# Optimization experiments

Hardware: AMD Instinct MI355X
Metric: run time of the kernel (lower is better)

The kernel has to match this reference:

```python
import jax, jax.numpy as jnp
import numpy as np

NUM_HEADS = 32
NUM_KV = 8
HEAD_DIM = 128


def rotate_half(x):
    half = x.shape[-1] // 2
    x1, x2 = x[..., :half], x[..., half:]
    return jnp.concatenate([-x2, x1], axis=-1)


def apply_rope(x, cos, sin):
    # x: [B, H, S, D]; cos/sin: [S, D] broadcast over batch and heads
    return x * cos + rotate_half(x) * sin


def setup_inputs() -> dict:
    key = jax.random.key(0)
    kx, kqkv, kout = jax.random.split(key, 3)
    B, S, H = 2, 2048, 4096
    x = jax.random.normal(kx, (B, S, H), dtype=jnp.float32)
    Wqkv = jax.random.normal(kqkv, (H, NUM_HEADS * HEAD_DIM + 2 * NUM_KV * HEAD_DIM), dtype=jnp.float32) * (H ** -0.5)
    Wout = jax.random.normal(kout, (H, H), dtype=jnp.float32) * (H ** -0.5)
    # realistic RoPE tables (seq, head_dim)
    inv_freq = 1.0 / (10000.0 ** (np.arange(0, HEAD_DIM, 2, dtype=np.float32) / HEAD_DIM))
    freqs = np.outer(np.arange(S, dtype=np.float32), inv_freq)  # [S, D/2]
    emb = np.concatenate([freqs, freqs], axis=-1)  # [S, D]
    cos = jnp.asarray(np.cos(emb), dtype=jnp.float32)
    sin = jnp.asarray(np.sin(emb), dtype=jnp.float32)
    return {"x": x, "cos": cos, "sin": sin, "Wqkv": Wqkv, "Wout": Wout}


def reference(x, cos, sin, Wqkv, Wout):
    B, S, H = x.shape
    nh, nkv, hd = NUM_HEADS, NUM_KV, HEAD_DIM
    qkv = x @ Wqkv  # [B, S, (nh+2*nkv)*hd]
    q, k, v = jnp.split(qkv, [nh * hd, nh * hd + nkv * hd], axis=-1)
    q = q.reshape(B, S, nh, hd).transpose(0, 2, 1, 3)   # [B, nh, S, hd]
    k = k.reshape(B, S, nkv, hd).transpose(0, 2, 1, 3)  # [B, nkv, S, hd]
    v = v.reshape(B, S, nkv, hd).transpose(0, 2, 1, 3)
    q = apply_rope(q, cos, sin)
    k = apply_rope(k, cos, sin)
    group = nh // nkv
    k = jnp.repeat(k, group, axis=1)  # repeat_interleave over head dim
    v = jnp.repeat(v, group, axis=1)
    scale = 1.0 / jnp.sqrt(jnp.asarray(hd, dtype=x.dtype))
    scores = jnp.einsum('bhqd,bhkd->bhqk', q, k) * scale  # [B, nh, S, S]
    causal = jnp.triu(jnp.ones((S, S), dtype=bool), k=1)
    scores = jnp.where(causal, -jnp.inf, scores)
    w = jax.nn.softmax(scores, axis=-1)
    out = jnp.einsum('bhqk,bhkd->bhqd', w, v)  # [B, nh, S, hd]
    out = out.transpose(0, 2, 1, 3).reshape(B, S, nh * hd)
    return out @ Wout
```

## Files before the change

### kernel.cpp

```cpp
#include <hip/hip_runtime.h>

typedef unsigned short u16;
typedef __attribute__((ext_vector_type(8))) short s16x8;
typedef __attribute__((ext_vector_type(4))) short s16x4;
typedef __attribute__((ext_vector_type(4))) float f32x4;

#define DEVI __device__ __forceinline__

DEVI u16 f2b(float f) {
  union { float f; unsigned u; } v; v.f = f;
  unsigned r = v.u + 0x7FFFu + ((v.u >> 16) & 1u);
  return (u16)(r >> 16);
}
DEVI float b2f(u16 h) {
  union { unsigned u; float f; } v; v.u = ((unsigned)h) << 16;
  return v.f;
}

typedef const __attribute__((address_space(1))) void gas_void;
typedef __attribute__((address_space(3))) void las_void;
DEVI void gload16(const void* g, void* l) {
  __builtin_amdgcn_global_load_lds((gas_void*)g, (las_void*)l, 16, 0, 0);
}

__global__ void conv_bf16(const float* __restrict__ in, u16* __restrict__ out, int n8) {
  int i = blockIdx.x * 256 + threadIdx.x;
  if (i >= n8) return;
  const float* p = in + (size_t)i * 8;
  float4 u = *(const float4*)p;
  float4 v = *(const float4*)(p + 4);
  s16x8 o = {(short)f2b(u.x), (short)f2b(u.y), (short)f2b(u.z), (short)f2b(u.w),
             (short)f2b(v.x), (short)f2b(v.y), (short)f2b(v.z), (short)f2b(v.w)};
  *(s16x8*)(out + (size_t)i * 8) = o;
}

__global__ void trans_bf16(const float* __restrict__ W, u16* __restrict__ Wt, int K, int N) {
  __shared__ __attribute__((aligned(16))) u16 tile[64][68];
  const int t = threadIdx.x;
  const int n0 = blockIdx.x * 64, k0 = blockIdx.y * 64;
#pragma unroll
  for (int i = 0; i < 4; ++i) {
    int c = i * 256 + t;
    int r = c >> 4, q = c & 15;
    float4 v = *(const float4*)(W + (size_t)(k0 + r) * N + n0 + q * 4);
    s16x4 o = {(short)f2b(v.x), (short)f2b(v.y), (short)f2b(v.z), (short)f2b(v.w)};
    *(s16x4*)&tile[r][q * 4] = o;
  }
  __syncthreads();
#pragma unroll
  for (int i = 0; i < 2; ++i) {
    int c = i * 256 + t;
    int n_ = c >> 3, ck = (c & 7) * 8;
    s16x8 o;
#pragma unroll
    for (int j = 0; j < 8; ++j) o[j] = (short)tile[ck + j][n_];
    *(s16x8*)(Wt + (size_t)(n0 + n_) * K + k0 + ck) = o;
  }
}

template <typename TC>
__global__ __launch_bounds__(512, 2) void gemm256(const u16* __restrict__ A,
                                                  const u16* __restrict__ Bt,
                                                  TC* __restrict__ C, int M, int N, int K) {
  __shared__ __attribute__((aligned(16))) u16 As[2][2][128 * 64];
  __shared__ __attribute__((aligned(16))) u16 Bs[2][2][128 * 64];
  const int t = threadIdx.x;
  const int nbn = N >> 8;
  const int nwg = (M >> 8) * nbn;
  const int chunk = nwg >> 3;
  const int id = (blockIdx.x & 7) * chunk + (blockIdx.x >> 3);
  const int row0 = (id / nbn) << 8, col0 = (id % nbn) << 8;
  const int w = t >> 6, lane = t & 63, lc = lane & 15, lg = lane >> 4;
  const int wqm = (w >> 2) * 64;
  const int wqn = (w & 3) * 32;
  const int sw7 = lc & 7;

  const f32x4 FZ = {0.f, 0.f, 0.f, 0.f};
  f32x4 acc[4][4][2];
#pragma unroll
  for (int q = 0; q < 4; ++q)
#pragma unroll
    for (int i = 0; i < 4; ++i)
#pragma unroll
      for (int j = 0; j < 2; ++j) acc[q][i][j] = FZ;

  const int s_r0 = t >> 3, s_r1 = (512 + t) >> 3;
  const int s_s = t & 7;

#define STG_A(kt, H, sl)                                                                   \
  {                                                                                        \
    gload16(A + (size_t)(row0 + (H)*128 + s_r0) * K + ((kt) << 6) + ((s_s ^ (s_r0 & 7)) << 3), \
            (u16*)As[sl][H] + t * 8);                                                      \
    gload16(A + (size_t)(row0 + (H)*128 + s_r1) * K + ((kt) << 6) + ((s_s ^ (s_r1 & 7)) << 3), \
            (u16*)As[sl][H] + (512 + t) * 8);                                              \
  }
#define STG_B(kt, H, sl)                                                                   \
  {                                                                                        \
    gload16(Bt + (size_t)(col0 + (H)*128 + s_r0) * K + ((kt) << 6) + ((s_s ^ (s_r0 & 7)) << 3), \
            (u16*)Bs[sl][H] + t * 8);                                                      \
    gload16(Bt + (size_t)(col0 + (H)*128 + s_r1) * K + ((kt) << 6) + ((s_s ^ (s_r1 & 7)) << 3), \
            (u16*)Bs[sl][H] + (512 + t) * 8);                                              \
  }
#define LOAD_A(MH, buf)                                                           \
  _Pragma("unroll") for (int mf = 0; mf < 4; ++mf)                                \
  _Pragma("unroll") for (int ks = 0; ks < 2; ++ks)                                \
    af[mf][ks] = *(const s16x8*)(As[buf][MH] + (wqm + mf * 16 + lc) * 64 +        \
                                 (((ks * 4 + lg) ^ sw7) << 3));
#define LOAD_B(NH, buf, DST)                                                      \
  _Pragma("unroll") for (int nf = 0; nf < 2; ++nf)                                \
  _Pragma("unroll") for (int ks = 0; ks < 2; ++ks)                                \
    DST[nf][ks] = *(const s16x8*)(Bs[buf][NH] + (wqn + nf * 16 + lc) * 64 +       \
                                  (((ks * 4 + lg) ^ sw7) << 3));
#define MFMA_Q(q, BV)                                                             \
  _Pragma("unroll") for (int ks = 0; ks < 2; ++ks)                                \
  _Pragma("unroll") for (int mf = 0; mf < 4; ++mf)                                \
  _Pragma("unroll") for (int nf = 0; nf < 2; ++nf)                                \
    acc[q][mf][nf] = __builtin_amdgcn_mfma_f32_16x16x32_bf16(                     \
        af[mf][ks], BV[nf][ks], acc[q][mf][nf], 0, 0, 0);
#define BAR __builtin_amdgcn_s_barrier()
#define PRIO1 __builtin_amdgcn_s_setprio(1)
#define PRIO0 __builtin_amdgcn_s_setprio(0)
#define WAIT6 asm volatile("s_waitcnt vmcnt(6)" ::: "memory")

  s16x8 af[4][2], bfv0[2][2], bfv1[2][2];
  const int NT = K >> 6, TM = NT - 1;

  STG_A(0, 0, 0) STG_B(0, 0, 0) STG_B(0, 1, 0) STG_A(0, 1, 0)
  STG_A(1, 0, 1) STG_B(1, 0, 1) STG_B(1, 1, 1)
  WAIT6;
  BAR;

  for (int kt = 0; kt < NT; ++kt) {
    const int buf = kt & 1, nb = buf ^ 1;
    const int tp1 = (kt + 1) & TM, tp2 = (kt + 2) & TM;
    LOAD_A(0, buf) LOAD_B(0, buf, bfv0)
    STG_A(tp1, 1, nb)
    BAR; PRIO1; MFMA_Q(0, bfv0) PRIO0; BAR;
    LOAD_B(1, buf, bfv1)
    STG_A(tp2, 0, buf)
    BAR; PRIO1; MFMA_Q(1, bfv1) PRIO0; BAR;
    LOAD_A(1, buf)
    STG_B(tp2, 0, buf)
    BAR; PRIO1; MFMA_Q(2, bfv1) PRIO0; BAR;
    STG_B(tp2, 1, buf)
    BAR; PRIO1; MFMA_Q(3, bfv0) PRIO0;
    WAIT6;
    BAR;
  }
  asm volatile("s_waitcnt vmcnt(0)" ::: "memory");
  BAR;
#undef STG_A
#undef STG_B
#undef LOAD_A
#undef LOAD_B
#undef MFMA_Q
#undef BAR
#undef PRIO1
#undef PRIO0
#undef WAIT6

  const int qmh[4] = {0, 0, 1, 1}, qnh[4] = {0, 1, 1, 0};
#pragma unroll
  for (int q = 0; q < 4; ++q)
#pragma unroll
    for (int mf = 0; mf < 4; ++mf)
#pragma unroll
      for (int nf = 0; nf < 2; ++nf)
#pragma unroll
        for (int r = 0; r < 4; ++r) {
          const int rg = row0 + qmh[q] * 128 + wqm + mf * 16 + lg * 4 + r;
          const int cg = col0 + qnh[q] * 128 + wqn + nf * 16 + lc;
          if constexpr (sizeof(TC) == 2)
            ((u16*)C)[(size_t)rg * N + cg] = f2b(acc[q][mf][nf][r]);
          else
            ((float*)C)[(size_t)rg * N + cg] = acc[q][mf][nf][r];
        }
}

__global__ void rope_kernel(u16* __restrict__ qkv, const float* __restrict__ cosb,
                            const float* __restrict__ sinb) {
  const int bs = blockIdx.x;
  const int s = bs & 2047;
  u16* row = qkv + (size_t)bs * 6144;
  const float* cr = cosb + s * 128;
  const float* sr = sinb + s * 128;
  for (int p = threadIdx.x; p < 320; p += 256) {
    int head = p >> 3, dc = (p & 7) * 8;
    int ci = head * 128 + dc;
    s16x8 a = *(const s16x8*)&row[ci];
    s16x8 bb = *(const s16x8*)&row[ci + 64];
    float4 c0 = *(const float4*)(cr + dc), c1 = *(const float4*)(cr + dc + 4);
    float4 s0 = *(const float4*)(sr + dc), s1 = *(const float4*)(sr + dc + 4);
    float cv[8] = {c0.x, c0.y, c0.z, c0.w, c1.x, c1.y, c1.z, c1.w};
    float sv[8] = {s0.x, s0.y, s0.z, s0.w, s1.x, s1.y, s1.z, s1.w};
    s16x8 o1, o2;
#pragma unroll
    for (int j = 0; j < 8; ++j) {
      float x1 = b2f((u16)a[j]), x2 = b2f((u16)bb[j]);
      o1[j] = (short)f2b(x1 * cv[j] - x2 * sv[j]);
      o2[j] = (short)f2b(x2 * cv[j] + x1 * sv[j]);
    }
    *(s16x8*)&row[ci] = o1;
    *(s16x8*)&row[ci + 64] = o2;
  }
}

__global__ void vtrans_kernel(const u16* __restrict__ qkv, u16* __restrict__ v_t) {
  __shared__ __attribute__((aligned(16))) u16 tile[64][72];
  const int t = threadIdx.x;
  const int s0 = blockIdx.x * 64;
  const int d0 = blockIdx.y * 64;
  const int bk = blockIdx.z;
  const int b = bk >> 3, kvh = bk & 7;
  const int slot = t & 7, r0 = t >> 3;
#pragma unroll
  for (int i = 0; i < 2; ++i) {
    int s_ = r0 + 32 * i;
    *(s16x8*)&tile[s_][slot * 8] =
        *(const s16x8*)(qkv + (size_t)(b * 2048 + s0 + s_) * 6144 + 5120 + kvh * 128 + d0 + slot * 8);
  }
  __syncthreads();
#pragma unroll
  for (int i = 0; i < 2; ++i) {
    int d_ = r0 + 32 * i;
    s16x8 v;
#pragma unroll
    for (int j = 0; j < 8; ++j) v[j] = (short)tile[slot * 8 + j][d_];
    *(s16x8*)(v_t + ((size_t)bk * 128 + d0 + d_) * 2048 + s0 + slot * 8) = v;
  }
}

__global__ void __launch_bounds__(256, 2) attn_kernel(const u16* __restrict__ qkv,
                                                      const u16* __restrict__ v_t,
                                                      u16* __restrict__ attn) {
  __shared__ __attribute__((aligned(16))) u16 Ks[64][136];
  __shared__ __attribute__((aligned(16))) u16 Vs[128][72];
  __shared__ __attribute__((aligned(16))) u16 Ps[4][32][72];
  const int t = threadIdx.x;
  const int f = blockIdx.x;
  const int xcd = f & 7, ix = f >> 3;
  const int g = (xcd << 1) | (ix >> 6);
  const int r_ = ix & 63;
  const int b = g >> 3, kvh = g & 7;
  const int qt = 15 - (r_ >> 2);
  const int h = kvh * 4 + (r_ & 3);
  const int q0 = qt * 128;
  const int w = t >> 6, lane = t & 63, lc = lane & 15, lg = lane >> 4;
  const int qw = q0 + w * 32;

  const u16* qbase = qkv + (size_t)(b * 2048) * 6144 + h * 128;
  const u16* kbase = qkv + (size_t)(b * 2048) * 6144 + 4096 + kvh * 128;
  const u16* vbase = v_t + (size_t)(b * 8 + kvh) * 128 * 2048;

  s16x8 qf[2][4];
#pragma unroll
  for (int mf = 0; mf < 2; ++mf)
#pragma unroll
    for (int ks = 0; ks < 4; ++ks)
      qf[mf][ks] = *(const s16x8*)(qbase + (size_t)(qw + mf * 16 + lc) * 6144 + ks * 32 + lg * 8);

  const f32x4 FZ = {0.f, 0.f, 0.f, 0.f};
  f32x4 o_acc[2][8];
  float m_run[2][4], l_run[2][4];
#pragma unroll
  for (int mf = 0; mf < 2; ++mf) {
#pragma unroll
    for (int nf = 0; nf < 8; ++nf) o_acc[mf][nf] = FZ;
#pragma unroll
    for (int r = 0; r < 4; ++r) { m_run[mf][r] = -3e38f; l_run[mf][r] = 0.f; }
  }
  const float scale2 = 0.08838834764831845f * 1.44269504088896340736f;

  const int ntiles = q0 / 64 + 2;
  s16x8 kr[4], vr[4];
#pragma unroll
  for (int i = 0; i < 4; ++i) {
    int c = i * 256 + t;
    kr[i] = *(const s16x8*)(kbase + (size_t)(c >> 4) * 6144 + (c & 15) * 8);
    vr[i] = *(const s16x8*)(vbase + (size_t)(c >> 3) * 2048 + (c & 7) * 8);
  }

  for (int kt = 0; kt < ntiles; ++kt) {
    const int k0 = kt * 64;
    __syncthreads();
#pragma unroll
    for (int i = 0; i < 4; ++i) {
      int c = i * 256 + t;
      *(s16x8*)&Ks[c >> 4][(c & 15) * 8] = kr[i];
      *(s16x8*)&Vs[c >> 3][(c & 7) * 8] = vr[i];
    }
    __syncthreads();
    if (kt + 1 < ntiles) {
      int k1 = k0 + 64;
#pragma unroll
      for (int i = 0; i < 4; ++i) {
        int c = i * 256 + t;
        kr[i] = *(const s16x8*)(kbase + (size_t)(k1 + (c >> 4)) * 6144 + (c & 15) * 8);
        vr[i] = *(const s16x8*)(vbase + (size_t)(c >> 3) * 2048 + k1 + (c & 7) * 8);
      }
    }
    if (k0 > qw + 31) continue;

    f32x4 sacc[2][4];
#pragma unroll
    for (int mf = 0; mf < 2; ++mf)
#pragma unroll
      for (int nf = 0; nf < 4; ++nf) sacc[mf][nf] = FZ;
#pragma unroll
    for (int ks = 0; ks < 4; ++ks) {
      s16x8 kf[4];
#pragma unroll
      for (int nf = 0; nf < 4; ++nf)
        kf[nf] = *(const s16x8*)&Ks[nf * 16 + lc][ks * 32 + lg * 8];
#pragma unroll
      for (int mf = 0; mf < 2; ++mf)
#pragma unroll
        for (int nf = 0; nf < 4; ++nf)
          sacc[mf][nf] = __builtin_amdgcn_mfma_f32_16x16x32_bf16(qf[mf][ks], kf[nf], sacc[mf][nf], 0, 0, 0);
    }

#pragma unroll
    for (int mf = 0; mf < 2; ++mf) {
      float pm[4] = {-3e38f, -3e38f, -3e38f, -3e38f};
      const bool dm = (k0 + 63 > qw + mf * 16);
      if (dm) {
#pragma unroll
        for (int nf = 0; nf < 4; ++nf) {
          int kv = k0 + nf * 16 + lc;
#pragma unroll
          for (int r = 0; r < 4; ++r) {
            int qg = qw + mf * 16 + lg * 4 + r;
            float sv = sacc[mf][nf][r] * scale2;
            sv = (kv <= qg) ? sv : -3e38f;
            sacc[mf][nf][r] = sv;
            pm[r] = fmaxf(pm[r], sv);
          }
        }
      } else {
#pragma unroll
        for (int nf = 0; nf < 4; ++nf)
#pragma unroll
          for (int r = 0; r < 4; ++r) {
            float sv = sacc[mf][nf][r] * scale2;
            sacc[mf][nf][r] = sv;
            pm[r] = fmaxf(pm[r], sv);
          }
      }
#pragma unroll
      for (int r = 0; r < 4; ++r) {
        pm[r] = fmaxf(pm[r], __shfl_xor(pm[r], 1));
        pm[r] = fmaxf(pm[r], __shfl_xor(pm[r], 2));
        pm[r] = fmaxf(pm[r], __shfl_xor(pm[r], 4));
        pm[r] = fmaxf(pm[r], __shfl_xor(pm[r], 8));
      }
      bool any = false;
      float mnew[4];
#pragma unroll
      for (int r = 0; r < 4; ++r) {
        mnew[r] = fmaxf(m_run[mf][r], pm[r]);
        any |= (mnew[r] > m_run[mf][r]);
      }
      if (__any(any)) {
#pragma unroll
        for (int r = 0; r < 4; ++r) {
          float fsc = exp2f(m_run[mf][r] - mnew[r]);
          m_run[mf][r] = mnew[r];
          l_run[mf][r] *= fsc;
#pragma unroll
          for (int nf = 0; nf < 8; ++nf) o_acc[mf][nf][r] *= fsc;
        }
      }
      float psum[4] = {0.f, 0.f, 0.f, 0.f};
#pragma unroll
      for (int nf = 0; nf < 4; ++nf)
#pragma unroll
        for (int r = 0; r < 4; ++r) {
          float p = exp2f(sacc[mf][nf][r] - m_run[mf][r]);
          psum[r] += p;
          Ps[w][mf * 16 + lg * 4 + r][nf * 16 + lc] = f2b(p);
        }
#pragma unroll
      for (int r = 0; r < 4; ++r) {
        float ps = psum[r];
        ps += __shfl_xor(ps, 1);
        ps += __shfl_xor(ps, 2);
        ps += __shfl_xor(ps, 4);
        ps += __shfl_xor(ps, 8);
        l_run[mf][r] += ps;
      }
    }
#pragma unroll
    for (int ks = 0; ks < 2; ++ks) {
      s16x8 pf[2];
#pragma unroll
      for (int mf = 0; mf < 2; ++mf)
        pf[mf] = *(const s16x8*)&Ps[w][mf * 16 + lc][ks * 32 + lg * 8];
#pragma unroll
      for (int nf = 0; nf < 8; ++nf) {
        s16x8 vf = *(const s16x8*)&Vs[nf * 16 + lc][ks * 32 + lg * 8];
#pragma unroll
        for (int mf = 0; mf < 2; ++mf)
          o_acc[mf][nf] = __builtin_amdgcn_mfma_f32_16x16x32_bf16(pf[mf], vf, o_acc[mf][nf], 0, 0, 0);
      }
    }
  }

#pragma unroll
  for (int mf = 0; mf < 2; ++mf)
#pragma unroll
    for (int r = 0; r < 4; ++r) {
      float inv = 1.0f / l_run[mf][r];
      int qg = qw + mf * 16 + lg * 4 + r;
#pragma unroll
      for (int nf = 0; nf < 8; ++nf)
        attn[(size_t)(b * 2048 + qg) * 4096 + h * 128 + nf * 16 + lc] =
            f2b(o_acc[mf][nf][r] * inv);
    }
}

extern "C" void kernel_launch(void* const* d_in, const int* in_sizes, int n_in,
                              void* d_out, int out_size, void* d_ws, size_t ws_size,
                              hipStream_t stream) {
  (void)in_sizes; (void)n_in; (void)out_size; (void)ws_size;
  const float* x = (const float*)d_in[0];
  const float* cosb = (const float*)d_in[1];
  const float* sinb = (const float*)d_in[2];
  const float* Wqkv = (const float*)d_in[3];
  const float* Wout = (const float*)d_in[4];
  float* out = (float*)d_out;
  char* ws = (char*)d_ws;

  u16* buf0 = (u16*)ws;
  u16* buf1 = (u16*)(ws + 50331648);
  u16* regc = (u16*)(ws + 100663296);

  conv_bf16<<<8192, 256, 0, stream>>>(x, regc, 2097152);
  trans_bf16<<<dim3(96, 64), 256, 0, stream>>>(Wqkv, buf0, 4096, 6144);
  gemm256<u16><<<384, 512, 0, stream>>>(regc, buf0, buf1, 4096, 6144, 4096);
  rope_kernel<<<4096, 256, 0, stream>>>(buf1, cosb, sinb);
  vtrans_kernel<<<dim3(32, 2, 16), 256, 0, stream>>>(buf1, regc);
  attn_kernel<<<1024, 256, 0, stream>>>(buf1, regc, buf0);
  trans_bf16<<<dim3(64, 64), 256, 0, stream>>>(Wout, regc, 4096, 4096);
  gemm256<float><<<256, 512, 0, stream>>>(buf0, regc, out, 4096, 4096, 4096);
}
```

Before: 567.8 us.

## Add 128x256-tile GEMM kernel for the QKV projection to fix wave quantization

Adds a new gemm128 kernel that computes 128x256 output tiles instead of 256x256, and uses it for the QKV projection. This raises the launch from 384 to 768 workgroups. The aim is to reduce tail waste, since 384 large tiles do not fill the CUs evenly. The B tile is staged in two 128-column halves with interleaved MFMA phases and double-buffered LDS. The trade-off is lower arithmetic intensity per tile and more redundant B loads.

```diff
diff --git a/kernel.cpp b/kernel.cpp
--- a/kernel.cpp
+++ b/kernel.cpp
@@ -56,6 +56,114 @@
     for (int j = 0; j < 8; ++j) o[j] = (short)tile[ck + j][n_];
     *(s16x8*)(Wt + (size_t)(n0 + n_) * K + k0 + ck) = o;
   }
+}
+
+template <typename TC>
+__global__ __launch_bounds__(512, 2) void gemm128(const u16* __restrict__ A,
+                                                  const u16* __restrict__ Bt,
+                                                  TC* __restrict__ C, int M, int N, int K) {
+  __shared__ __attribute__((aligned(16))) u16 As[2][128 * 64];
+  __shared__ __attribute__((aligned(16))) u16 Bs[2][256 * 64];
+  const int t = threadIdx.x;
+  const int nbn = N >> 8;
+  const int nwg = (M >> 7) * nbn;
+  const int chunk = nwg >> 3;
+  const int id = (blockIdx.x & 7) * chunk + (blockIdx.x >> 3);
+  const int row0 = (id / nbn) << 7, col0 = (id % nbn) << 8;
+  const int w = t >> 6, lane = t & 63, lc = lane & 15, lg = lane >> 4;
+  const int wm = (w >> 2) * 64;
+  const int wn4 = (w & 3);
+  const int sw7 = lc & 7;
+
+  const f32x4 FZ = {0.f, 0.f, 0.f, 0.f};
+  f32x4 acc[4][4];
+#pragma unroll
+  for (int i = 0; i < 4; ++i)
+#pragma unroll
+    for (int j = 0; j < 4; ++j) acc[i][j] = FZ;
+
+  const int ra = t >> 3;
+  const int sa = (t & 7) ^ (ra & 7);
+  const int bg0 = ((ra >> 5) << 6) | (ra & 31);
+
+#define G1_STG_A(kt, sl)                                                          \
+  {                                                                               \
+    const u16* ap = A + (size_t)(row0 + ra) * K + ((kt) << 6) + (sa << 3);        \
+    gload16(ap, (u16*)As[sl] + t * 8);                                            \
+    gload16(ap + (size_t)64 * K, (u16*)As[sl] + (512 + t) * 8);                   \
+  }
+#define G1_STG_B(kt, H, sl)                                                       \
+  {                                                                               \
+    const u16* bp = Bt + (size_t)(col0 + bg0 + ((H) << 5)) * K + ((kt) << 6) + (sa << 3); \
+    gload16(bp, (u16*)Bs[sl] + (H)*8192 + t * 8);                                 \
+    gload16(bp + (size_t)128 * K, (u16*)Bs[sl] + (H)*8192 + (512 + t) * 8);       \
+  }
+#define G1_LOAD_A(buf)                                                            \
+  _Pragma("unroll") for (int mf = 0; mf < 4; ++mf)                                \
+  _Pragma("unroll") for (int ks = 0; ks < 2; ++ks)                                \
+    af[mf][ks] = *(const s16x8*)(As[buf] + (wm + mf * 16 + lc) * 64 +             \
+                                 (((ks * 4 + lg) ^ sw7) << 3));
+#define G1_LOAD_B(NH, buf)                                                        \
+  _Pragma("unroll") for (int nfl = 0; nfl < 2; ++nfl)                             \
+  _Pragma("unroll") for (int ks = 0; ks < 2; ++ks)                                \
+    bfv[nfl][ks] = *(const s16x8*)(Bs[buf] + ((NH)*128 + wn4 * 32 + nfl * 16 + lc) * 64 + \
+                                   (((ks * 4 + lg) ^ sw7) << 3));
+#define G1_MFMA(NH)                                                               \
+  _Pragma("unroll") for (int ks = 0; ks < 2; ++ks)                                \
+  _Pragma("unroll") for (int mf = 0; mf < 4; ++mf)                                \
+  _Pragma("unroll") for (int nfl = 0; nfl < 2; ++nfl)                             \
+    acc[mf][(NH)*2 + nfl] = __builtin_amdgcn_mfma_f32_16x16x32_bf16(              \
+        af[mf][ks], bfv[nfl][ks], acc[mf][(NH)*2 + nfl], 0, 0, 0);
+#define BAR __builtin_amdgcn_s_barrier()
+#define PRIO1 __builtin_amdgcn_s_setprio(1)
+#define PRIO0 __builtin_amdgcn_s_setprio(0)
+
+  s16x8 af[4][2], bfv[2][2];
+  const int NT = K >> 6, TM = NT - 1;
+
+  G1_STG_A(0, 0) G1_STG_B(0, 0, 0) G1_STG_B(0, 1, 0)
+  asm volatile("s_waitcnt vmcnt(2)" ::: "memory");
+  BAR;
+
+  for (int kt = 0; kt < NT; ++kt) {
+    const int buf = kt & 1, nb = buf ^ 1;
+    const int tp1 = (kt + 1) & TM;
+    G1_LOAD_A(buf)
+    G1_LOAD_B(0, buf)
+    G1_STG_A(tp1, nb)
+    G1_STG_B(tp1, 0, nb)
+    BAR; PRIO1; G1_MFMA(0) PRIO0;
+    asm volatile("s_waitcnt vmcnt(4)" ::: "memory");
+    BAR;
+    G1_LOAD_B(1, buf)
+    G1_STG_B(tp1, 1, nb)
+    BAR; PRIO1; G1_MFMA(1) PRIO0;
+    asm volatile("s_waitcnt vmcnt(2)" ::: "memory");
+    BAR;
+  }
+  asm volatile("s_waitcnt vmcnt(0)" ::: "memory");
+#undef G1_STG_A
+#undef G1_STG_B
+#undef G1_LOAD_A
+#undef G1_LOAD_B
+#undef G1_MFMA
+#undef BAR
+#undef PRIO1
+#undef PRIO0
+
+#pragma unroll
+  for (int mf = 0; mf < 4; ++mf)
+#pragma unroll
+    for (int nf = 0; nf < 4; ++nf)
+#pragma unroll
+      for (int r = 0; r < 4; ++r) {
+        const int rg = row0 + wm + mf * 16 + lg * 4 + r;
+        const int cg = col0 + wn4 * 64 + (nf >> 1) * 32 + (nf & 1) * 16 + lc;
+        if constexpr (sizeof(TC) == 2)
+          ((u16*)C)[(size_t)rg * N + cg] = f2b(acc[mf][nf][r]);
+        else
+          ((float*)C)[(size_t)rg * N + cg] = acc[mf][nf][r];
+      }
 }
 
 template <typename TC>
@@ -436,7 +544,7 @@
 
   conv_bf16<<<8192, 256, 0, stream>>>(x, regc, 2097152);
   trans_bf16<<<dim3(96, 64), 256, 0, stream>>>(Wqkv, buf0, 4096, 6144);
-  gemm256<u16><<<384, 512, 0, stream>>>(regc, buf0, buf1, 4096, 6144, 4096);
+  gemm128<u16><<<768, 512, 0, stream>>>(regc, buf0, buf1, 4096, 6144, 4096);
   rope_kernel<<<4096, 256, 0, stream>>>(buf1, cosb, sinb);
   vtrans_kernel<<<dim3(32, 2, 16), 256, 0, stream>>>(buf1, regc);
   attn_kernel<<<1024, 256, 0, stream>>>(buf1, regc, buf0);
```

After: 564.7 us. No clear change (-0.5%).
